# Kernel optimization log

Hardware: AMD Instinct MI355X
Metric: run time of the kernel (lower is better)

Reference implementation:

```python
import jax, jax.numpy as jnp
import numpy as np

NEG = -1e30  # finite stand-in for -inf so grads stay clean
BLANK = 0


def _ctc_single(lp, tgt, il, tl):
    """CTC negative log-likelihood for one example.
    lp: (T, C) log-probs, tgt: (S,) labels, il/tl: scalar lengths."""
    T, C = lp.shape
    S = tgt.shape[0]
    L = 2 * S + 1  # extended label sequence: blank, t0, blank, t1, ...
    s_idx = jnp.arange(L)
    ext = jnp.where(s_idx % 2 == 0, BLANK, tgt[jnp.minimum(s_idx // 2, S - 1)])
    ext_prev2 = jnp.concatenate([jnp.full((2,), -1, ext.dtype), ext[:-2]])
    allow2 = (s_idx % 2 == 1) & (ext != ext_prev2)  # skip transition allowed
    valid = s_idx < 2 * tl + 1  # mask lattice positions beyond this target

    lp_ext = lp[:, ext]  # (T, L) gather of log-probs onto the lattice

    alpha0 = jnp.full((L,), NEG, lp.dtype)
    alpha0 = alpha0.at[0].set(lp_ext[0, 0])
    alpha0 = alpha0.at[1].set(jnp.where(tl > 0, lp_ext[0, 1], NEG))
    alpha0 = jnp.where(valid, alpha0, NEG)

    def step(alpha, lp_t):
        a1 = alpha
        a2 = jnp.concatenate([jnp.full((1,), NEG, alpha.dtype), alpha[:-1]])
        a3 = jnp.where(allow2,
                       jnp.concatenate([jnp.full((2,), NEG, alpha.dtype), alpha[:-2]]),
                       NEG)
        m = jnp.maximum(a1, jnp.maximum(a2, a3))
        lse = m + jnp.log(jnp.exp(a1 - m) + jnp.exp(a2 - m) + jnp.exp(a3 - m))
        new = jnp.where(valid, lse + lp_t, NEG)
        return new, new

    _, alphas = jax.lax.scan(step, alpha0, lp_ext[1:])
    alphas = jnp.concatenate([alpha0[None], alphas], axis=0)  # (T, L)

    a_fin = alphas[il - 1]
    end1 = a_fin[2 * tl]  # final blank
    end2 = jnp.where(tl > 0, a_fin[jnp.maximum(2 * tl - 1, 0)], NEG)  # final label
    m = jnp.maximum(end1, end2)
    ll = m + jnp.log(jnp.exp(end1 - m) + jnp.exp(end2 - m))
    return -ll


def ctc_loss(log_probs, targets, input_lengths, target_lengths):
    # log_probs: (T, N, C); vmap over the batch axis
    losses = jax.vmap(_ctc_single, in_axes=(1, 0, 0, 0))(
        log_probs, targets, input_lengths, target_lengths)
    # zero_infinity=True: zero out non-finite (huge) losses
    losses = jnp.where(losses >= 1e29, 0.0, losses)
    # reduction='mean': per-example loss divided by target length, then batch mean
    denom = jnp.maximum(target_lengths, 1).astype(losses.dtype)
    return jnp.mean(losses / denom)


def setup_inputs() -> dict:
    key = jax.random.key(0)
    k1, k2 = jax.random.split(key)
    T, N, C, S = 512, 32, 5000, 128
    logits = jax.random.normal(k1, (T, N, C), dtype=jnp.float32)
    log_probs = jax.nn.log_softmax(logits, axis=-1)
    # labels in [1, C): blank index 0 must not appear in targets
    targets = jax.random.randint(k2, (N, S), 1, C, dtype=jnp.int32)
    input_lengths = jnp.full((N,), T, dtype=jnp.int32)
    target_lengths = jnp.full((N,), S, dtype=jnp.int32)
    return {"log_probs": log_probs, "targets": targets,
            "input_lengths": input_lengths, "target_lengths": target_lengths}


def reference(log_probs, targets, input_lengths, target_lengths):
    return ctc_loss(log_probs, targets, input_lengths, target_lengths)
```

## Files before the change

kernel.cpp:

```cpp
#include <hip/hip_runtime.h>

#define T_DIM 512
#define N_DIM 32
#define C_DIM 5000
#define S_DIM 128
#define STRIDE_T (N_DIM * C_DIM)

#define CROW 130
#define TOTAL_G (T_DIM * N_DIM * 129)
#define GBLK 1024
#define GTHR 256
#define GSTRIDE (GBLK * GTHR)
#define GPT 9

#define TC 64
#define NCHUNK (T_DIM / TC)
#define CH2 (TC * (CROW / 2))
#define NLOADERS 192
#define NLOADF2 22

#define NEGF (-1e30f)
#define LOG2E_F 1.4426950408889634f
#define LN2_F 0.6931471805599453f

__device__ __forceinline__ float fexp2(float x) {
#if __has_builtin(__builtin_amdgcn_exp2f)
    return __builtin_amdgcn_exp2f(x);
#else
    return exp2f(x);
#endif
}
__device__ __forceinline__ float flog2(float x) {
#if __has_builtin(__builtin_amdgcn_logf)
    return __builtin_amdgcn_logf(x);
#else
    return log2f(x);
#endif
}

__device__ __forceinline__ float lse2(float a, float b) {
    float m = fmaxf(a, b);
    return m + flog2(fexp2(a - m) + fexp2(b - m));
}
__device__ __forceinline__ float lse3(float a, float b, float c) {
    float m = fmaxf(a, fmaxf(b, c));
    return m + flog2(fexp2(a - m) + fexp2(b - m) + fexp2(c - m));
}

__global__ __launch_bounds__(GTHR, 4) void ctc_gather_kernel(
        const float* __restrict__ lp,
        const int* __restrict__ tgt,
        float* __restrict__ compact)
{
    const int tid0 = blockIdx.x * GTHR + threadIdx.x;
    float vals[GPT];
    int   outi[GPT];
#pragma unroll
    for (int j = 0; j < GPT; ++j) {
        int i = tid0 + GSTRIDE * j;
        const int ic = (i < TOTAL_G) ? i : (TOTAL_G - 1);
        const int q = ic / 129;
        const int k = ic - q * 129;
        const int nb = q >> 9;
        const int t = q & 511;
        const int cls = (k < 128) ? tgt[nb * S_DIM + k] : 0;
        vals[j] = lp[(size_t)t * STRIDE_T + nb * C_DIM + cls];
        outi[j] = (i < TOTAL_G) ? (q * CROW + k) : -1;
    }
#pragma unroll
    for (int j = 0; j < GPT; ++j) {
        if (outi[j] >= 0) compact[(size_t)outi[j]] = vals[j];
    }
}

__global__ __launch_bounds__(256, 1) void ctc_scan_kernel(
        const float* __restrict__ compact,
        const int* __restrict__ tgt,
        const int* __restrict__ il,
        const int* __restrict__ tl,
        float* __restrict__ loss_out)
{
    const int n = blockIdx.x;
    const int tid = threadIdx.x;
    const int wid = tid >> 6;
    const int lane = tid & 63;

    const int tlen = tl[n];
    const int ilen = il[n];
    const int* tgn = tgt + n * S_DIM;
    const float2* cbase2 = (const float2*)(compact + (size_t)n * T_DIM * CROW);

    __shared__ float buf[2][TC * CROW];
    __shared__ float sh[2];

    if (wid != 0) {
        const int ltid = tid - 64;
        float2* dst2 = (float2*)buf[0];
        float2 rg[NLOADF2];
#pragma unroll
        for (int j = 0; j < NLOADF2; ++j) {
            int i2 = ltid + NLOADERS * j;
            if (i2 >= CH2) i2 = CH2 - 1;
            rg[j] = cbase2[i2];
        }
#pragma unroll
        for (int j = 0; j < NLOADF2; ++j) {
            int i2 = ltid + NLOADERS * j;
            if (i2 >= CH2) i2 = CH2 - 1;
            dst2[i2] = rg[j];
        }
    }

    const int c1i = 2 * lane;
    const int c3i = 2 * lane + 1;
    bool allow2_1 = false, allow2_3 = false;
    if (wid == 0) {
        const int c1 = tgn[c1i];
        const int c3 = tgn[c3i];
        const int c1prev = (c1i > 0) ? tgn[c1i - 1] : -1;
        allow2_1 = (c1i > 0) && (c1 != c1prev);
        allow2_3 = (c3 != c1);
    }
    const int vmax = 2 * tlen;
    const int sb = lane << 2;
    const bool v0 = (sb    ) <= vmax;
    const bool v1 = (sb + 1) <= vmax;
    const bool v2 = (sb + 2) <= vmax;
    const bool v3 = (sb + 3) <= vmax;
    const bool v4 = (lane == 63) && (256 <= vmax);
    const int e1s = 2 * tlen;
    const int e2s = (2 * tlen - 1 > 0) ? (2 * tlen - 1) : 0;

    float a0 = NEGF, a1 = NEGF, a2 = NEGF, a3 = NEGF, a4 = NEGF;

    __syncthreads();

    for (int cc = 0; cc < NCHUNK; ++cc) {
        if (wid != 0) {
            if (cc + 1 < NCHUNK) {
                const int ltid = tid - 64;
                const float2* src2 = cbase2 + (size_t)(cc + 1) * CH2;
                float2* dst2 = (float2*)buf[(cc + 1) & 1];
                float2 rg[NLOADF2];
#pragma unroll
                for (int j = 0; j < NLOADF2; ++j) {
                    int i2 = ltid + NLOADERS * j;
                    if (i2 >= CH2) i2 = CH2 - 1;
                    rg[j] = src2[i2];
                }
#pragma unroll
                for (int j = 0; j < NLOADF2; ++j) {
                    int i2 = ltid + NLOADERS * j;
                    if (i2 >= CH2) i2 = CH2 - 1;
                    dst2[i2] = rg[j];
                }
            }
        } else {
            const float* lb = buf[cc & 1];
            float2 pq = *(const float2*)&lb[0 * CROW + 2 * lane];
            float pbv = lb[0 * CROW + 128];
#pragma unroll 8
            for (int tt = 0; tt < TC; ++tt) {
                const int ttn = (tt + 1 < TC) ? (tt + 1) : tt;
                const float2 pq_n = *(const float2*)&lb[ttn * CROW + 2 * lane];
                const float pbv_n = lb[ttn * CROW + 128];

                const int t = cc * TC + tt;
                const float pb = pbv  * LOG2E_F;
                const float p1 = pq.x * LOG2E_F;
                const float p3 = pq.y * LOG2E_F;

                if (t == 0) {
                    a0 = (lane == 0) ? pb : NEGF;
                    a1 = (lane == 0 && tlen > 0) ? p1 : NEGF;
                    a2 = NEGF; a3 = NEGF; a4 = NEGF;
                    a0 = v0 ? a0 : NEGF;
                    a1 = v1 ? a1 : NEGF;
                } else {
                    float am1 = __shfl_up(a3, 1);
                    if (lane == 0) am1 = NEGF;

                    const float n0 = lse2(a0, am1);
                    const float n1 = allow2_1 ? lse3(a1, a0, am1) : lse2(a1, a0);
                    const float n2 = lse2(a2, a1);
                    const float n3 = allow2_3 ? lse3(a3, a2, a1) : lse2(a3, a2);
                    const float n4 = lse2(a4, a3);

                    a0 = v0 ? (n0 + pb) : NEGF;
                    a1 = v1 ? (n1 + p1) : NEGF;
                    a2 = v2 ? (n2 + pb) : NEGF;
                    a3 = v3 ? (n3 + p3) : NEGF;
                    a4 = v4 ? (n4 + pb) : NEGF;
                }

                if (t == ilen - 1) {
                    if (sb     == e1s) sh[0] = a0;
                    if (sb + 1 == e1s) sh[0] = a1;
                    if (sb + 2 == e1s) sh[0] = a2;
                    if (sb + 3 == e1s) sh[0] = a3;
                    if (lane == 63 && e1s == 256) sh[0] = a4;
                    if (sb     == e2s) sh[1] = a0;
                    if (sb + 1 == e2s) sh[1] = a1;
                    if (sb + 2 == e2s) sh[1] = a2;
                    if (sb + 3 == e2s) sh[1] = a3;
                }

                pq = pq_n; pbv = pbv_n;
            }
        }
        __syncthreads();
    }

    if (tid == 0) {
        const float e1 = sh[0];
        const float e2 = (tlen > 0) ? sh[1] : NEGF;
        const float m = fmaxf(e1, e2);
        const float ll2 = m + flog2(fexp2(e1 - m) + fexp2(e2 - m));
        const float ll = ll2 * LN2_F;
        float loss = -ll;
        if (loss >= 1e29f) loss = 0.f;
        const int denom = (tlen > 1) ? tlen : 1;
        loss_out[n] = loss / (float)denom;
    }
}

#define FLDW 132
#define FNLOADERS 192
#define FNLOAD ((TC * 129) / FNLOADERS)

__global__ __launch_bounds__(256, 1) void ctc_fused_kernel(
        const float* __restrict__ lp, const int* __restrict__ tgt,
        const int* __restrict__ il, const int* __restrict__ tl,
        float* __restrict__ loss_out)
{
    const int n = blockIdx.x;
    const int tid = threadIdx.x;
    const int wid = tid >> 6;
    const int lane = tid & 63;
    const int tlen = tl[n];
    const int ilen = il[n];
    const int* tgn = tgt + n * S_DIM;
    const float* base = lp + (size_t)n * C_DIM;
    __shared__ float buf[2][TC * FLDW];
    __shared__ float sh[2];
    int gof[FNLOAD]; int wo[FNLOAD];
    if (wid != 0) {
        const int ltid = tid - 64;
#pragma unroll
        for (int j = 0; j < FNLOAD; ++j) {
            const int i = ltid + FNLOADERS * j;
            const int t = i / 129;
            const int k = i - 129 * t;
            const int cls = (k < 128) ? tgn[k] : 0;
            gof[j] = t * STRIDE_T + cls;
            wo[j] = t * FLDW + k;
        }
        float rg[FNLOAD];
#pragma unroll
        for (int j = 0; j < FNLOAD; ++j) rg[j] = base[(size_t)gof[j]];
#pragma unroll
        for (int j = 0; j < FNLOAD; ++j) buf[0][wo[j]] = rg[j];
    }
    const int c1i = 2 * lane;
    const int c3i = 2 * lane + 1;
    bool allow2_1 = false, allow2_3 = false;
    if (wid == 0) {
        const int c1 = tgn[c1i];
        const int c3 = tgn[c3i];
        const int c1prev = (c1i > 0) ? tgn[c1i - 1] : -1;
        allow2_1 = (c1i > 0) && (c1 != c1prev);
        allow2_3 = (c3 != c1);
    }
    const int vmax = 2 * tlen;
    const int sb = lane << 2;
    const bool v0 = (sb) <= vmax, v1 = (sb+1) <= vmax, v2 = (sb+2) <= vmax, v3 = (sb+3) <= vmax;
    const bool v4 = (lane == 63) && (256 <= vmax);
    const int e1s = 2 * tlen;
    const int e2s = (2 * tlen - 1 > 0) ? (2 * tlen - 1) : 0;
    float a0 = NEGF, a1 = NEGF, a2 = NEGF, a3 = NEGF, a4 = NEGF;
    __syncthreads();
    for (int cc = 0; cc < NCHUNK; ++cc) {
        if (wid != 0) {
            if (cc + 1 < NCHUNK) {
                const float* bp = base + (size_t)(cc + 1) * TC * STRIDE_T;
                float* dst = buf[(cc + 1) & 1];
                float rg[FNLOAD];
#pragma unroll
                for (int j = 0; j < FNLOAD; ++j) rg[j] = bp[(size_t)gof[j]];
#pragma unroll
                for (int j = 0; j < FNLOAD; ++j) dst[wo[j]] = rg[j];
            }
        } else {
            const float* lb = buf[cc & 1];
            float2 pq = *(const float2*)&lb[0 * FLDW + 2 * lane];
            float pbv = lb[0 * FLDW + 128];
#pragma unroll 8
            for (int tt = 0; tt < TC; ++tt) {
                const int ttn = (tt + 1 < TC) ? (tt + 1) : tt;
                const float2 pq_n = *(const float2*)&lb[ttn * FLDW + 2 * lane];
                const float pbv_n = lb[ttn * FLDW + 128];
                const int t = cc * TC + tt;
                const float pb = pbv * LOG2E_F, p1 = pq.x * LOG2E_F, p3 = pq.y * LOG2E_F;
                if (t == 0) {
                    a0 = (lane == 0) ? pb : NEGF;
                    a1 = (lane == 0 && tlen > 0) ? p1 : NEGF;
                    a2 = NEGF; a3 = NEGF; a4 = NEGF;
                    a0 = v0 ? a0 : NEGF;
                    a1 = v1 ? a1 : NEGF;
                } else {
                    float am1 = __shfl_up(a3, 1);
                    if (lane == 0) am1 = NEGF;
                    const float n0 = lse2(a0, am1);
                    const float n1 = allow2_1 ? lse3(a1, a0, am1) : lse2(a1, a0);
                    const float n2 = lse2(a2, a1);
                    const float n3 = allow2_3 ? lse3(a3, a2, a1) : lse2(a3, a2);
                    const float n4 = lse2(a4, a3);
                    a0 = v0 ? (n0 + pb) : NEGF;
                    a1 = v1 ? (n1 + p1) : NEGF;
                    a2 = v2 ? (n2 + pb) : NEGF;
                    a3 = v3 ? (n3 + p3) : NEGF;
                    a4 = v4 ? (n4 + pb) : NEGF;
                }
                if (t == ilen - 1) {
                    if (sb     == e1s) sh[0] = a0;
                    if (sb + 1 == e1s) sh[0] = a1;
                    if (sb + 2 == e1s) sh[0] = a2;
                    if (sb + 3 == e1s) sh[0] = a3;
                    if (lane == 63 && e1s == 256) sh[0] = a4;
                    if (sb     == e2s) sh[1] = a0;
                    if (sb + 1 == e2s) sh[1] = a1;
                    if (sb + 2 == e2s) sh[1] = a2;
                    if (sb + 3 == e2s) sh[1] = a3;
                }
                pq = pq_n; pbv = pbv_n;
            }
        }
        __syncthreads();
    }
    if (tid == 0) {
        const float e1 = sh[0];
        const float e2 = (tlen > 0) ? sh[1] : NEGF;
        const float m = fmaxf(e1, e2);
        const float ll2 = m + flog2(fexp2(e1 - m) + fexp2(e2 - m));
        float loss = -(ll2 * LN2_F);
        if (loss >= 1e29f) loss = 0.f;
        const int denom = (tlen > 1) ? tlen : 1;
        loss_out[n] = loss / (float)denom;
    }
}

__global__ __launch_bounds__(64, 1) void ctc_reduce_kernel(
        const float* __restrict__ loss, float* __restrict__ out)
{
    const int lane = threadIdx.x;
    float v = (lane < N_DIM) ? loss[lane] : 0.f;
#pragma unroll
    for (int off = 32; off > 0; off >>= 1) v += __shfl_down(v, off);
    if (lane == 0) out[0] = v / (float)N_DIM;
}

extern "C" void kernel_launch(void* const* d_in, const int* in_sizes, int n_in,
                              void* d_out, int out_size, void* d_ws, size_t ws_size,
                              hipStream_t stream) {
    const float* lp = (const float*)d_in[0];
    const int* tgt = (const int*)d_in[1];
    const int* il = (const int*)d_in[2];
    const int* tl = (const int*)d_in[3];
    float* out = (float*)d_out;
    float* losses = (float*)d_ws;
    float* compact = (float*)((char*)d_ws + 512);

    const size_t need = 512 + (size_t)N_DIM * T_DIM * CROW * sizeof(float);
    if (ws_size >= need) {
        ctc_gather_kernel<<<GBLK, GTHR, 0, stream>>>(lp, tgt, compact);
        ctc_scan_kernel<<<N_DIM, 256, 0, stream>>>(compact, tgt, il, tl, losses);
    } else {
        ctc_fused_kernel<<<N_DIM, 256, 0, stream>>>(lp, tgt, il, tl, losses);
    }
    ctc_reduce_kernel<<<1, 64, 0, stream>>>(losses, out);
}
```

Measured before the change: 156.6 us.

## Replace random-gather of lattice log-probs with class-map streaming filter

Builds a per-example class-to-slot byte map, then streams each full (t,n) row of log-probs with coalesced float4 loads and scatters only the target classes into a compact buffer. This replaces the scattered 4-byte gathers of the earlier gather kernel. The scan kernel now reads through first-occurrence slot indices, so duplicate labels share one compact column. It reads the whole 327 MB log-prob tensor instead of only the needed entries, trading extra bandwidth for coalescing, and adds a kernel launch.

```diff
diff --git a/kernel.cpp b/kernel.cpp
--- a/kernel.cpp
+++ b/kernel.cpp
@@ -7,11 +7,17 @@
 #define STRIDE_T (N_DIM * C_DIM)
 
 #define CROW 130
-#define TOTAL_G (T_DIM * N_DIM * 129)
-#define GBLK 1024
-#define GTHR 256
-#define GSTRIDE (GBLK * GTHR)
-#define GPT 9
+#define MAPB 5008
+
+#define OFF_LOSS 0
+#define OFF_MAP 512
+#define OFF_FS (OFF_MAP + N_DIM * MAPB)
+#define OFF_COMPACT (OFF_FS + N_DIM * S_DIM)
+#define WS_NEED (OFF_COMPACT + (size_t)N_DIM * T_DIM * CROW * 4)
+
+#define FT 8
+#define FBLK ((T_DIM / FT) * N_DIM)
+#define C4 (C_DIM / 4)
 
 #define TC 64
 #define NCHUNK (T_DIM / TC)
@@ -37,7 +43,6 @@
     return log2f(x);
 #endif
 }
-
 __device__ __forceinline__ float lse2(float a, float b) {
     float m = fmaxf(a, b);
     return m + flog2(fexp2(a - m) + fexp2(b - m));
@@ -47,37 +52,66 @@
     return m + flog2(fexp2(a - m) + fexp2(b - m) + fexp2(c - m));
 }
 
-__global__ __launch_bounds__(GTHR, 4) void ctc_gather_kernel(
+__global__ __launch_bounds__(256, 1) void ctc_mapbuild_kernel(
+        const int* __restrict__ tgt,
+        unsigned char* __restrict__ map,
+        unsigned char* __restrict__ fs)
+{
+    const int n = blockIdx.x;
+    const int tid = threadIdx.x;
+    __shared__ unsigned char smap[MAPB];
+    __shared__ int scls[S_DIM];
+    for (int i = tid; i < MAPB / 4; i += 256) ((unsigned int*)smap)[i] = 0xFFFFFFFFu;
+    if (tid < S_DIM) scls[tid] = tgt[n * S_DIM + tid];
+    __syncthreads();
+    if (tid == 0) {
+        smap[0] = 128;
+        for (int k = S_DIM - 1; k >= 0; --k) smap[scls[k]] = (unsigned char)k;
+    }
+    __syncthreads();
+    unsigned int* gmap = (unsigned int*)(map + n * MAPB);
+    for (int i = tid; i < MAPB / 4; i += 256) gmap[i] = ((const unsigned int*)smap)[i];
+    if (tid < S_DIM) fs[n * S_DIM + tid] = smap[scls[tid]];
+}
+
+__global__ __launch_bounds__(256, 8) void ctc_filter_kernel(
         const float* __restrict__ lp,
-        const int* __restrict__ tgt,
+        const unsigned char* __restrict__ map,
         float* __restrict__ compact)
 {
-    const int tid0 = blockIdx.x * GTHR + threadIdx.x;
-    float vals[GPT];
-    int   outi[GPT];
-#pragma unroll
-    for (int j = 0; j < GPT; ++j) {
-        int i = tid0 + GSTRIDE * j;
-        const int ic = (i < TOTAL_G) ? i : (TOTAL_G - 1);
-        const int q = ic / 129;
-        const int k = ic - q * 129;
-        const int nb = q >> 9;
-        const int t = q & 511;
-        const int cls = (k < 128) ? tgt[nb * S_DIM + k] : 0;
-        vals[j] = lp[(size_t)t * STRIDE_T + nb * C_DIM + cls];
-        outi[j] = (i < TOTAL_G) ? (q * CROW + k) : -1;
-    }
-#pragma unroll
-    for (int j = 0; j < GPT; ++j) {
-        if (outi[j] >= 0) compact[(size_t)outi[j]] = vals[j];
+    const int bid = blockIdx.x;
+    const int n = bid & (N_DIM - 1);
+    const int tb = (bid >> 5) * FT;
+    const int tid = threadIdx.x;
+
+    __shared__ unsigned int smap[MAPB / 4];
+    const unsigned int* gmap = (const unsigned int*)(map + n * MAPB);
+    for (int i = tid; i < MAPB / 4; i += 256) smap[i] = gmap[i];
+    __syncthreads();
+
+    for (int t = tb; t < tb + FT; ++t) {
+        const float4* row = (const float4*)(lp + (size_t)t * STRIDE_T + n * C_DIM);
+        float* crow = compact + ((size_t)n * T_DIM + t) * CROW;
+        for (int i = tid; i < C4; i += 256) {
+            const float4 v = row[i];
+            const unsigned int mm = smap[i];
+            if (mm != 0xFFFFFFFFu) {
+                const unsigned s0 = mm & 255u, s1 = (mm >> 8) & 255u;
+                const unsigned s2 = (mm >> 16) & 255u, s3 = mm >> 24;
+                if (s0 != 255u) crow[s0] = v.x;
+                if (s1 != 255u) crow[s1] = v.y;
+                if (s2 != 255u) crow[s2] = v.z;
+                if (s3 != 255u) crow[s3] = v.w;
+            }
+        }
     }
 }
 
 __global__ __launch_bounds__(256, 1) void ctc_scan_kernel(
         const float* __restrict__ compact,
         const int* __restrict__ tgt,
-        const int* __restrict__ il,
-        const int* __restrict__ tl,
+        const unsigned char* __restrict__ fs,
+        const int* __restrict__ il, const int* __restrict__ tl,
         float* __restrict__ loss_out)
 {
     const int n = blockIdx.x;
@@ -99,27 +133,27 @@
         float2 rg[NLOADF2];
 #pragma unroll
         for (int j = 0; j < NLOADF2; ++j) {
-            int i2 = ltid + NLOADERS * j;
-            if (i2 >= CH2) i2 = CH2 - 1;
+            int i2 = ltid + NLOADERS * j; if (i2 >= CH2) i2 = CH2 - 1;
             rg[j] = cbase2[i2];
         }
 #pragma unroll
         for (int j = 0; j < NLOADF2; ++j) {
-            int i2 = ltid + NLOADERS * j;
-            if (i2 >= CH2) i2 = CH2 - 1;
+            int i2 = ltid + NLOADERS * j; if (i2 >= CH2) i2 = CH2 - 1;
             dst2[i2] = rg[j];
         }
     }
 
-    const int c1i = 2 * lane;
-    const int c3i = 2 * lane + 1;
+    int r1 = 0, r3 = 0;
     bool allow2_1 = false, allow2_3 = false;
     if (wid == 0) {
+        const int c1i = 2 * lane, c3i = 2 * lane + 1;
         const int c1 = tgn[c1i];
         const int c3 = tgn[c3i];
         const int c1prev = (c1i > 0) ? tgn[c1i - 1] : -1;
         allow2_1 = (c1i > 0) && (c1 != c1prev);
         allow2_3 = (c3 != c1);
+        r1 = fs[n * S_DIM + c1i];
+        r3 = fs[n * S_DIM + c3i];
     }
     const int vmax = 2 * tlen;
     const int sb = lane << 2;
@@ -144,31 +178,29 @@
                 float2 rg[NLOADF2];
 #pragma unroll
                 for (int j = 0; j < NLOADF2; ++j) {
-                    int i2 = ltid + NLOADERS * j;
-                    if (i2 >= CH2) i2 = CH2 - 1;
+                    int i2 = ltid + NLOADERS * j; if (i2 >= CH2) i2 = CH2 - 1;
                     rg[j] = src2[i2];
                 }
 #pragma unroll
                 for (int j = 0; j < NLOADF2; ++j) {
-                    int i2 = ltid + NLOADERS * j;
-                    if (i2 >= CH2) i2 = CH2 - 1;
+                    int i2 = ltid + NLOADERS * j; if (i2 >= CH2) i2 = CH2 - 1;
                     dst2[i2] = rg[j];
                 }
             }
         } else {
             const float* lb = buf[cc & 1];
-            float2 pq = *(const float2*)&lb[0 * CROW + 2 * lane];
-            float pbv = lb[0 * CROW + 128];
+            float p1v = lb[r1], p3v = lb[r3], pbv = lb[128];
 #pragma unroll 8
             for (int tt = 0; tt < TC; ++tt) {
                 const int ttn = (tt + 1 < TC) ? (tt + 1) : tt;
-                const float2 pq_n = *(const float2*)&lb[ttn * CROW + 2 * lane];
-                const float pbv_n = lb[ttn * CROW + 128];
+                const float p1n = lb[ttn * CROW + r1];
+                const float p3n = lb[ttn * CROW + r3];
+                const float pbn = lb[ttn * CROW + 128];
 
                 const int t = cc * TC + tt;
-                const float pb = pbv  * LOG2E_F;
-                const float p1 = pq.x * LOG2E_F;
-                const float p3 = pq.y * LOG2E_F;
+                const float pb = pbv * LOG2E_F;
+                const float p1 = p1v * LOG2E_F;
+                const float p3 = p3v * LOG2E_F;
 
                 if (t == 0) {
                     a0 = (lane == 0) ? pb : NEGF;
@@ -204,8 +236,7 @@
                     if (sb + 2 == e2s) sh[1] = a2;
                     if (sb + 3 == e2s) sh[1] = a3;
                 }
-
-                pq = pq_n; pbv = pbv_n;
+                p1v = p1n; p3v = p3n; pbv = pbn;
             }
         }
         __syncthreads();
@@ -216,8 +247,7 @@
         const float e2 = (tlen > 0) ? sh[1] : NEGF;
         const float m = fmaxf(e1, e2);
         const float ll2 = m + flog2(fexp2(e1 - m) + fexp2(e2 - m));
-        const float ll = ll2 * LN2_F;
-        float loss = -ll;
+        float loss = -(ll2 * LN2_F);
         if (loss >= 1e29f) loss = 0.f;
         const int denom = (tlen > 1) ? tlen : 1;
         loss_out[n] = loss / (float)denom;
@@ -261,8 +291,7 @@
 #pragma unroll
         for (int j = 0; j < FNLOAD; ++j) buf[0][wo[j]] = rg[j];
     }
-    const int c1i = 2 * lane;
-    const int c3i = 2 * lane + 1;
+    const int c1i = 2 * lane, c3i = 2 * lane + 1;
     bool allow2_1 = false, allow2_3 = false;
     if (wid == 0) {
         const int c1 = tgn[c1i];
@@ -367,13 +396,16 @@
     const int* il = (const int*)d_in[2];
     const int* tl = (const int*)d_in[3];
     float* out = (float*)d_out;
-    float* losses = (float*)d_ws;
-    float* compact = (float*)((char*)d_ws + 512);
-
-    const size_t need = 512 + (size_t)N_DIM * T_DIM * CROW * sizeof(float);
-    if (ws_size >= need) {
-        ctc_gather_kernel<<<GBLK, GTHR, 0, stream>>>(lp, tgt, compact);
-        ctc_scan_kernel<<<N_DIM, 256, 0, stream>>>(compact, tgt, il, tl, losses);
+
+    float* losses = (float*)((char*)d_ws + OFF_LOSS);
+    unsigned char* map = (unsigned char*)d_ws + OFF_MAP;
+    unsigned char* fs = (unsigned char*)d_ws + OFF_FS;
+    float* compact = (float*)((char*)d_ws + OFF_COMPACT);
+
+    if (ws_size >= WS_NEED) {
+        ctc_mapbuild_kernel<<<N_DIM, 256, 0, stream>>>(tgt, map, fs);
+        ctc_filter_kernel<<<FBLK, 256, 0, stream>>>(lp, map, compact);
+        ctc_scan_kernel<<<N_DIM, 256, 0, stream>>>(compact, tgt, fs, il, tl, losses);
     } else {
         ctc_fused_kernel<<<N_DIM, 256, 0, stream>>>(lp, tgt, il, tl, losses);
     }
```

After: 181.7 us. 16.0% more time.
